# Performance work log

Measured on AMD Instinct MI355X. Metric: run time of the kernel, lower is better.

Reference implementation:

```python
import jax, jax.numpy as jnp
import numpy as np

B, L, D = 4, 4096, 1024
LN_EPS = 1e-5
SCAN_EPS = 1e-8


def setup_inputs() -> dict:
    key = jax.random.key(0)
    ks = jax.random.split(key, 5)
    s = 1.0 / np.sqrt(D)
    return {
        "X": jax.random.normal(ks[0], (B, L, D), dtype=jnp.float32),
        "Wa": jax.random.normal(ks[1], (D, D), dtype=jnp.float32) * s,
        "ba": jnp.zeros((D,), dtype=jnp.float32),
        "Wb": jax.random.normal(ks[2], (D, D), dtype=jnp.float32) * s,
        "bb": jnp.zeros((D,), dtype=jnp.float32),
        "Wc": jax.random.normal(ks[3], (D, D), dtype=jnp.float32) * s,
        "bc": jnp.zeros((D,), dtype=jnp.float32),
        "gamma": jnp.ones((D,), dtype=jnp.float32),
        "beta": jnp.zeros((D,), dtype=jnp.float32),
        "h0": jax.random.normal(ks[4], (1, D), dtype=jnp.float32),
    }


def reference(X, Wa, ba, Wb, bb, Wc, bc, gamma, beta, h0):
    # LayerNorm over last dim
    mu = jnp.mean(X, axis=-1, keepdims=True)
    var = jnp.mean(jnp.square(X - mu), axis=-1, keepdims=True)
    Z = (X - mu) * jax.lax.rsqrt(var + LN_EPS) * gamma + beta  # [B,L,D]

    A = jax.nn.sigmoid(jnp.einsum("bld,ed->ble", Z, Wa) + ba)   # gate in (0,1)
    P = jnp.cumprod(A, axis=1)                                   # decay products
    Bx = jnp.einsum("bld,ed->ble", Z, Wb) + bb
    S = jnp.cumsum(Bx / (P + SCAN_EPS), axis=1)
    # h_t = P_t * h0 + P_t * sum_{s<=t} Bx_s / P_s   (linear recurrence)
    h = P * (h0[:, None, :] + S)                                 # h0 [1,D] broadcasts
    C = jnp.einsum("bld,ed->ble", Z, Wc) + bc
    return C * h + X  # dropout is identity at inference
```

## Files before the change

kernel.cpp:

```cpp
#include <hip/hip_runtime.h>
#include <hip/hip_bf16.h>
#include <cstdint>
#include <cstddef>

#define B_ 4
#define L_ 4096
#define D_ 1024
#define M_ (B_ * L_)
#define LN_EPS 1e-5f
#define SCAN_EPS 1e-8f
#define CT 64
#define NC (L_ / CT)

typedef float f32x4 __attribute__((ext_vector_type(4)));
typedef short bf16x8 __attribute__((ext_vector_type(8)));

__device__ __forceinline__ void gload_lds16(const void* g, void* l) {
    __builtin_amdgcn_global_load_lds(
        (const __attribute__((address_space(1))) void*)g,
        (__attribute__((address_space(3))) void*)l, 16, 0, 0);
}

__global__ __launch_bounds__(256) void ln_kernel(
    const float* __restrict__ X, const float* __restrict__ gamma,
    const float* __restrict__ beta, __hip_bfloat16* __restrict__ Zb)
{
    const int row = blockIdx.x;
    const int tid = threadIdx.x;
    const float* x = X + (size_t)row * D_;

    float4 v = *reinterpret_cast<const float4*>(x + tid * 4);
    float s = v.x + v.y + v.z + v.w;
    #pragma unroll
    for (int off = 32; off > 0; off >>= 1) s += __shfl_down(s, off);

    __shared__ float red[4];
    __shared__ float red2[4];
    const int wid = tid >> 6, lane = tid & 63;
    if (lane == 0) red[wid] = s;
    __syncthreads();
    const float mean = (red[0] + red[1] + red[2] + red[3]) * (1.0f / D_);

    const float dx = v.x - mean, dy = v.y - mean, dz = v.z - mean, dw = v.w - mean;
    float s2 = dx * dx + dy * dy + dz * dz + dw * dw;
    #pragma unroll
    for (int off = 32; off > 0; off >>= 1) s2 += __shfl_down(s2, off);
    if (lane == 0) red2[wid] = s2;
    __syncthreads();
    const float var = (red2[0] + red2[1] + red2[2] + red2[3]) * (1.0f / D_);
    const float rs = rsqrtf(var + LN_EPS);

    float4 g  = *reinterpret_cast<const float4*>(gamma + tid * 4);
    float4 be = *reinterpret_cast<const float4*>(beta + tid * 4);
    union { ushort4 u4; __hip_bfloat16 h[4]; } pk;
    pk.h[0] = __float2bfloat16(dx * rs * g.x + be.x);
    pk.h[1] = __float2bfloat16(dy * rs * g.y + be.y);
    pk.h[2] = __float2bfloat16(dz * rs * g.z + be.z);
    pk.h[3] = __float2bfloat16(dw * rs * g.w + be.w);
    *reinterpret_cast<ushort4*>(Zb + (size_t)row * D_ + tid * 4) = pk.u4;
}

__global__ __launch_bounds__(256) void cvt_w3(
    const float* __restrict__ Wa, const float* __restrict__ Wb,
    const float* __restrict__ Wc, __hip_bfloat16* __restrict__ Wbf)
{
    const int gid = blockIdx.x * 256 + threadIdx.x;
    const size_t i = (size_t)gid * 8;
    const int which = (int)(i >> 20);
    const size_t off = i & ((1ull << 20) - 1);
    const float* W = (which == 0) ? Wa : (which == 1) ? Wb : Wc;
    float4 v0 = *reinterpret_cast<const float4*>(W + off);
    float4 v1 = *reinterpret_cast<const float4*>(W + off + 4);
    union { bf16x8 v; __hip_bfloat16 h[8]; } pk;
    pk.h[0] = __float2bfloat16(v0.x); pk.h[1] = __float2bfloat16(v0.y);
    pk.h[2] = __float2bfloat16(v0.z); pk.h[3] = __float2bfloat16(v0.w);
    pk.h[4] = __float2bfloat16(v1.x); pk.h[5] = __float2bfloat16(v1.y);
    pk.h[6] = __float2bfloat16(v1.z); pk.h[7] = __float2bfloat16(v1.w);
    *reinterpret_cast<bf16x8*>(Wbf + i) = pk.v;
}

#define TM 128
#define TN 128
#define TK 32

__global__ __launch_bounds__(256) void gemm3_mfma(
    const __hip_bfloat16* __restrict__ Zb, const __hip_bfloat16* __restrict__ Wbf,
    const float* __restrict__ ba, const float* __restrict__ bb, const float* __restrict__ bc,
    __hip_bfloat16* __restrict__ Aout, __hip_bfloat16* __restrict__ Bxout,
    __hip_bfloat16* __restrict__ Cout, float* __restrict__ LP)
{
    __shared__ __hip_bfloat16 As[TM * TK];
    __shared__ __hip_bfloat16 Bs[TN * TK];

    const int tid  = threadIdx.x;
    const int wv   = tid >> 6;
    const int lane = tid & 63;
    const int wr   = wv >> 1, wc = wv & 1;
    const int m0   = blockIdx.y * TM;
    const int n0g  = blockIdx.x * TN;
    const int which = n0g >> 10;
    const int n0   = n0g & 1023;

    const __hip_bfloat16* __restrict__ Wsrc = Wbf + ((size_t)which << 20);
    const float* __restrict__ bias = (which == 0) ? ba : (which == 1) ? bb : bc;

    const int c0 = tid, c1 = 256 + tid;
    const int row0 = c0 >> 2, sc0 = (c0 & 3) ^ ((row0 >> 1) & 3);
    const int row1 = c1 >> 2, sc1 = (c1 & 3) ^ ((row1 >> 1) & 3);
    __hip_bfloat16* aDst0 = As + (size_t)(wv * 64) * 8;
    __hip_bfloat16* aDst1 = As + (size_t)(256 + wv * 64) * 8;
    __hip_bfloat16* bDst0 = Bs + (size_t)(wv * 64) * 8;
    __hip_bfloat16* bDst1 = Bs + (size_t)(256 + wv * 64) * 8;

    f32x4 acc[4][4] = {};

    for (int k0 = 0; k0 < D_; k0 += TK) {
        __syncthreads();
        gload_lds16(Zb   + (size_t)(m0 + row0) * D_ + k0 + sc0 * 8, aDst0);
        gload_lds16(Zb   + (size_t)(m0 + row1) * D_ + k0 + sc1 * 8, aDst1);
        gload_lds16(Wsrc + (size_t)(n0 + row0) * D_ + k0 + sc0 * 8, bDst0);
        gload_lds16(Wsrc + (size_t)(n0 + row1) * D_ + k0 + sc1 * 8, bDst1);
        __syncthreads();

        bf16x8 af[4], bfr[4];
        const int rl = lane & 15, kg = lane >> 4;
        #pragma unroll
        for (int i = 0; i < 4; ++i) {
            const int ra = wr * 64 + i * 16 + rl;
            af[i] = *reinterpret_cast<const bf16x8*>(
                reinterpret_cast<const char*>(As) + ra * 64 + ((kg ^ ((ra >> 1) & 3)) << 4));
            const int rb = wc * 64 + i * 16 + rl;
            bfr[i] = *reinterpret_cast<const bf16x8*>(
                reinterpret_cast<const char*>(Bs) + rb * 64 + ((kg ^ ((rb >> 1) & 3)) << 4));
        }
        #pragma unroll
        for (int i = 0; i < 4; ++i)
            #pragma unroll
            for (int j = 0; j < 4; ++j)
                acc[i][j] = __builtin_amdgcn_mfma_f32_16x16x32_bf16(
                    af[i], bfr[j], acc[i][j], 0, 0, 0);
    }

    const int cn = n0 + wc * 64 + (lane & 15);
    float bj[4];
    #pragma unroll
    for (int j = 0; j < 4; ++j) bj[j] = bias[cn + j * 16];

    if (which == 0) {
        float pp[4] = {1.0f, 1.0f, 1.0f, 1.0f};
        #pragma unroll
        for (int i = 0; i < 4; ++i) {
            #pragma unroll
            for (int r = 0; r < 4; ++r) {
                const int m = m0 + wr * 64 + i * 16 + (lane >> 4) * 4 + r;
                __hip_bfloat16* dst = Aout + (size_t)m * D_ + cn;
                #pragma unroll
                for (int j = 0; j < 4; ++j) {
                    const float val = 1.0f / (1.0f + expf(-(acc[i][j][r] + bj[j])));
                    const __hip_bfloat16 hb = __float2bfloat16(val);
                    dst[j * 16] = hb;
                    pp[j] *= __bfloat162float(hb);
                }
            }
        }
        #pragma unroll
        for (int j = 0; j < 4; ++j) {
            pp[j] *= __shfl_xor(pp[j], 16);
            pp[j] *= __shfl_xor(pp[j], 32);
        }
        const int rl = lane & 15, kg = lane >> 4;
        const float sel = (kg == 0) ? pp[0] : (kg == 1) ? pp[1] : (kg == 2) ? pp[2] : pp[3];
        const int bseq = m0 >> 12;
        const int cidx = ((m0 & 4095) >> 6) + wr;
        LP[((size_t)bseq * NC + cidx) * D_ + n0 + wc * 64 + kg * 16 + rl] = sel;
    } else {
        __hip_bfloat16* __restrict__ Out = (which == 1) ? Bxout : Cout;
        #pragma unroll
        for (int i = 0; i < 4; ++i) {
            #pragma unroll
            for (int r = 0; r < 4; ++r) {
                const int m = m0 + wr * 64 + i * 16 + (lane >> 4) * 4 + r;
                __hip_bfloat16* dst = Out + (size_t)m * D_ + cn;
                #pragma unroll
                for (int j = 0; j < 4; ++j)
                    dst[j * 16] = __float2bfloat16(acc[i][j][r] + bj[j]);
            }
        }
    }
}

__global__ __launch_bounds__(256) void scan_chunkpfx(
    const float* __restrict__ LP, float* __restrict__ Pstart)
{
    const int id = blockIdx.x * 256 + threadIdx.x;
    const int e = id & (D_ - 1);
    const int b = id >> 10;
    const size_t base = (size_t)b * NC * D_ + e;
    float p = 1.0f;
    for (int c = 0; c < NC; ++c) {
        Pstart[base + (size_t)c * D_] = p;
        p *= LP[base + (size_t)c * D_];
    }
}

__global__ __launch_bounds__(256) void scan_chunksum(
    const __hip_bfloat16* __restrict__ A, const __hip_bfloat16* __restrict__ Bx,
    const float* __restrict__ Pstart, float* __restrict__ Ssum)
{
    const int id = blockIdx.x * 256 + threadIdx.x;
    const int e = id & (D_ - 1);
    const int c = (id >> 10) & (NC - 1);
    const int b = id >> 16;
    size_t base = ((size_t)b * L_ + (size_t)c * CT) * D_ + e;
    float p = Pstart[id];
    float s = 0.0f;
    #pragma unroll 4
    for (int t = 0; t < CT; ++t) {
        const size_t idx = base + (size_t)t * D_;
        p *= __bfloat162float(A[idx]);
        s += __bfloat162float(Bx[idx]) / (p + SCAN_EPS);
    }
    Ssum[id] = s;
}

__global__ __launch_bounds__(256) void scan_sumpfx(
    const float* __restrict__ Ssum, float* __restrict__ Sstart)
{
    const int id = blockIdx.x * 256 + threadIdx.x;
    const int e = id & (D_ - 1);
    const int b = id >> 10;
    const size_t base = (size_t)b * NC * D_ + e;
    float s = 0.0f;
    for (int c = 0; c < NC; ++c) {
        Sstart[base + (size_t)c * D_] = s;
        s += Ssum[base + (size_t)c * D_];
    }
}

__global__ __launch_bounds__(256) void scan_final(
    const __hip_bfloat16* __restrict__ A, const __hip_bfloat16* __restrict__ Bx,
    const __hip_bfloat16* __restrict__ C, const float* __restrict__ X,
    const float* __restrict__ Pstart, const float* __restrict__ Sstart,
    const float* __restrict__ h0, float* __restrict__ out)
{
    const int id = blockIdx.x * 256 + threadIdx.x;
    const int e = id & (D_ - 1);
    const int c = (id >> 10) & (NC - 1);
    const int b = id >> 16;
    size_t base = ((size_t)b * L_ + (size_t)c * CT) * D_ + e;
    float p = Pstart[id];
    float s = Sstart[id];
    const float h0e = h0[e];
    #pragma unroll 4
    for (int t = 0; t < CT; ++t) {
        const size_t idx = base + (size_t)t * D_;
        p *= __bfloat162float(A[idx]);
        s += __bfloat162float(Bx[idx]) / (p + SCAN_EPS);
        const float h = p * (h0e + s);
        out[idx] = fmaf(__bfloat162float(C[idx]), h, X[idx]);
    }
}

extern "C" void kernel_launch(void* const* d_in, const int* in_sizes, int n_in,
                              void* d_out, int out_size, void* d_ws, size_t ws_size,
                              hipStream_t stream)
{
    const float* X     = (const float*)d_in[0];
    const float* Wa    = (const float*)d_in[1];
    const float* ba    = (const float*)d_in[2];
    const float* Wb    = (const float*)d_in[3];
    const float* bb    = (const float*)d_in[4];
    const float* Wc    = (const float*)d_in[5];
    const float* bc    = (const float*)d_in[6];
    const float* gamma = (const float*)d_in[7];
    const float* beta  = (const float*)d_in[8];
    const float* h0    = (const float*)d_in[9];
    float* out = (float*)d_out;

    const size_t NELT = (size_t)M_ * D_;
    const size_t NCH  = (size_t)B_ * NC * D_;

    __hip_bfloat16* Zb   = (__hip_bfloat16*)d_ws;
    __hip_bfloat16* Wbf  = Zb + NELT;
    __hip_bfloat16* Abf  = Wbf + 3ull * 1024 * 1024;
    __hip_bfloat16* Bxbf = Abf + NELT;
    __hip_bfloat16* Cbf  = Bxbf + NELT;
    float* LP   = (float*)(Cbf + NELT);
    float* Pst  = LP   + NCH;
    float* Ssum = Pst  + NCH;
    float* Sst  = Ssum + NCH;
    (void)ws_size; (void)in_sizes; (void)n_in; (void)out_size;

    cvt_w3<<<1536, 256, 0, stream>>>(Wa, Wb, Wc, Wbf);
    ln_kernel<<<M_, 256, 0, stream>>>(X, gamma, beta, Zb);

    gemm3_mfma<<<dim3(3072 / TN, M_ / TM), 256, 0, stream>>>(
        Zb, Wbf, ba, bb, bc, Abf, Bxbf, Cbf, LP);

    scan_chunkpfx<<<16, 256, 0, stream>>>(LP, Pst);
    scan_chunksum<<<1024, 256, 0, stream>>>(Abf, Bxbf, Pst, Ssum);
    scan_sumpfx<<<16, 256, 0, stream>>>(Ssum, Sst);
    scan_final<<<1024, 256, 0, stream>>>(Abf, Bxbf, Cbf, X, Pst, Sst, h0, out);
}
```

Measured before the change: 352.2 us.

## Double-buffer GEMM LDS, swizzle block order, fuse LN with weight cast, vectorize scans

The GEMM now double-buffers its LDS tiles and prefetches the next K slice before computing the current one, dropping one barrier per iteration. It also remaps a 1D grid so that consecutive blocks are spread across XCD-sized groups. LayerNorm switches to a single-pass sum and sum-of-squares reduction and is merged with the weight-conversion kernel into one launch. The scan kernels process two channels per thread with paired bf16 and float loads and use smaller blocks. The single-pass variance is less numerically robust, and double buffering doubles LDS use per block.

```diff
diff --git a/kernel.cpp b/kernel.cpp
--- a/kernel.cpp
+++ b/kernel.cpp
@@ -21,67 +21,69 @@
         (__attribute__((address_space(3))) void*)l, 16, 0, 0);
 }
 
-__global__ __launch_bounds__(256) void ln_kernel(
+__device__ __forceinline__ float bf2f(unsigned short u) {
+    return __uint_as_float((unsigned)u << 16);
+}
+
+__global__ __launch_bounds__(256) void ln_cvt_kernel(
     const float* __restrict__ X, const float* __restrict__ gamma,
-    const float* __restrict__ beta, __hip_bfloat16* __restrict__ Zb)
-{
+    const float* __restrict__ beta, __hip_bfloat16* __restrict__ Zb,
+    const float* __restrict__ Wa, const float* __restrict__ Wb,
+    const float* __restrict__ Wc, __hip_bfloat16* __restrict__ Wbf)
+{
+    const int tid = threadIdx.x;
+    if (blockIdx.x >= M_) {
+        const int gid = (blockIdx.x - M_) * 256 + tid;
+        const size_t i = (size_t)gid * 8;
+        const int which = (int)(i >> 20);
+        const size_t off = i & ((1ull << 20) - 1);
+        const float* W = (which == 0) ? Wa : (which == 1) ? Wb : Wc;
+        float4 v0 = *reinterpret_cast<const float4*>(W + off);
+        float4 v1 = *reinterpret_cast<const float4*>(W + off + 4);
+        union { bf16x8 v; __hip_bfloat16 h[8]; } pk;
+        pk.h[0] = __float2bfloat16(v0.x); pk.h[1] = __float2bfloat16(v0.y);
+        pk.h[2] = __float2bfloat16(v0.z); pk.h[3] = __float2bfloat16(v0.w);
+        pk.h[4] = __float2bfloat16(v1.x); pk.h[5] = __float2bfloat16(v1.y);
+        pk.h[6] = __float2bfloat16(v1.z); pk.h[7] = __float2bfloat16(v1.w);
+        *reinterpret_cast<bf16x8*>(Wbf + i) = pk.v;
+        return;
+    }
+
     const int row = blockIdx.x;
-    const int tid = threadIdx.x;
     const float* x = X + (size_t)row * D_;
 
     float4 v = *reinterpret_cast<const float4*>(x + tid * 4);
     float s = v.x + v.y + v.z + v.w;
+    float q = v.x * v.x + v.y * v.y + v.z * v.z + v.w * v.w;
     #pragma unroll
-    for (int off = 32; off > 0; off >>= 1) s += __shfl_down(s, off);
-
-    __shared__ float red[4];
-    __shared__ float red2[4];
+    for (int off = 32; off > 0; off >>= 1) {
+        s += __shfl_down(s, off);
+        q += __shfl_down(q, off);
+    }
+
+    __shared__ float red[8];
     const int wid = tid >> 6, lane = tid & 63;
-    if (lane == 0) red[wid] = s;
+    if (lane == 0) { red[wid] = s; red[4 + wid] = q; }
     __syncthreads();
     const float mean = (red[0] + red[1] + red[2] + red[3]) * (1.0f / D_);
-
-    const float dx = v.x - mean, dy = v.y - mean, dz = v.z - mean, dw = v.w - mean;
-    float s2 = dx * dx + dy * dy + dz * dz + dw * dw;
-    #pragma unroll
-    for (int off = 32; off > 0; off >>= 1) s2 += __shfl_down(s2, off);
-    if (lane == 0) red2[wid] = s2;
-    __syncthreads();
-    const float var = (red2[0] + red2[1] + red2[2] + red2[3]) * (1.0f / D_);
+    const float ex2  = (red[4] + red[5] + red[6] + red[7]) * (1.0f / D_);
+    const float var  = ex2 - mean * mean;
     const float rs = rsqrtf(var + LN_EPS);
 
     float4 g  = *reinterpret_cast<const float4*>(gamma + tid * 4);
     float4 be = *reinterpret_cast<const float4*>(beta + tid * 4);
     union { ushort4 u4; __hip_bfloat16 h[4]; } pk;
-    pk.h[0] = __float2bfloat16(dx * rs * g.x + be.x);
-    pk.h[1] = __float2bfloat16(dy * rs * g.y + be.y);
-    pk.h[2] = __float2bfloat16(dz * rs * g.z + be.z);
-    pk.h[3] = __float2bfloat16(dw * rs * g.w + be.w);
+    pk.h[0] = __float2bfloat16((v.x - mean) * rs * g.x + be.x);
+    pk.h[1] = __float2bfloat16((v.y - mean) * rs * g.y + be.y);
+    pk.h[2] = __float2bfloat16((v.z - mean) * rs * g.z + be.z);
+    pk.h[3] = __float2bfloat16((v.w - mean) * rs * g.w + be.w);
     *reinterpret_cast<ushort4*>(Zb + (size_t)row * D_ + tid * 4) = pk.u4;
-}
-
-__global__ __launch_bounds__(256) void cvt_w3(
-    const float* __restrict__ Wa, const float* __restrict__ Wb,
-    const float* __restrict__ Wc, __hip_bfloat16* __restrict__ Wbf)
-{
-    const int gid = blockIdx.x * 256 + threadIdx.x;
-    const size_t i = (size_t)gid * 8;
-    const int which = (int)(i >> 20);
-    const size_t off = i & ((1ull << 20) - 1);
-    const float* W = (which == 0) ? Wa : (which == 1) ? Wb : Wc;
-    float4 v0 = *reinterpret_cast<const float4*>(W + off);
-    float4 v1 = *reinterpret_cast<const float4*>(W + off + 4);
-    union { bf16x8 v; __hip_bfloat16 h[8]; } pk;
-    pk.h[0] = __float2bfloat16(v0.x); pk.h[1] = __float2bfloat16(v0.y);
-    pk.h[2] = __float2bfloat16(v0.z); pk.h[3] = __float2bfloat16(v0.w);
-    pk.h[4] = __float2bfloat16(v1.x); pk.h[5] = __float2bfloat16(v1.y);
-    pk.h[6] = __float2bfloat16(v1.z); pk.h[7] = __float2bfloat16(v1.w);
-    *reinterpret_cast<bf16x8*>(Wbf + i) = pk.v;
 }
 
 #define TM 128
 #define TN 128
 #define TK 32
+#define NKS (D_ / TK)
 
 __global__ __launch_bounds__(256) void gemm3_mfma(
     const __hip_bfloat16* __restrict__ Zb, const __hip_bfloat16* __restrict__ Wbf,
@@ -89,15 +91,20 @@
     __hip_bfloat16* __restrict__ Aout, __hip_bfloat16* __restrict__ Bxout,
     __hip_bfloat16* __restrict__ Cout, float* __restrict__ LP)
 {
-    __shared__ __hip_bfloat16 As[TM * TK];
-    __shared__ __hip_bfloat16 Bs[TN * TK];
+    __shared__ __hip_bfloat16 As[2][TM * TK];
+    __shared__ __hip_bfloat16 Bs[2][TN * TK];
 
     const int tid  = threadIdx.x;
     const int wv   = tid >> 6;
     const int lane = tid & 63;
     const int wr   = wv >> 1, wc = wv & 1;
-    const int m0   = blockIdx.y * TM;
-    const int n0g  = blockIdx.x * TN;
+
+    const int braw = blockIdx.x;
+    const int bid  = (braw & 7) * 384 + (braw >> 3);
+    const int nb   = bid % 24;
+    const int mb   = bid / 24;
+    const int m0   = mb * TM;
+    const int n0g  = nb * TN;
     const int which = n0g >> 10;
     const int n0   = n0g & 1023;
 
@@ -107,31 +114,42 @@
     const int c0 = tid, c1 = 256 + tid;
     const int row0 = c0 >> 2, sc0 = (c0 & 3) ^ ((row0 >> 1) & 3);
     const int row1 = c1 >> 2, sc1 = (c1 & 3) ^ ((row1 >> 1) & 3);
-    __hip_bfloat16* aDst0 = As + (size_t)(wv * 64) * 8;
-    __hip_bfloat16* aDst1 = As + (size_t)(256 + wv * 64) * 8;
-    __hip_bfloat16* bDst0 = Bs + (size_t)(wv * 64) * 8;
-    __hip_bfloat16* bDst1 = Bs + (size_t)(256 + wv * 64) * 8;
+    const int dOff0 = (wv * 64) * 8;
+    const int dOff1 = (256 + wv * 64) * 8;
+    const __hip_bfloat16* zSrc0 = Zb + (size_t)(m0 + row0) * D_ + sc0 * 8;
+    const __hip_bfloat16* zSrc1 = Zb + (size_t)(m0 + row1) * D_ + sc1 * 8;
+    const __hip_bfloat16* wSrc0 = Wsrc + (size_t)(n0 + row0) * D_ + sc0 * 8;
+    const __hip_bfloat16* wSrc1 = Wsrc + (size_t)(n0 + row1) * D_ + sc1 * 8;
 
     f32x4 acc[4][4] = {};
-
-    for (int k0 = 0; k0 < D_; k0 += TK) {
-        __syncthreads();
-        gload_lds16(Zb   + (size_t)(m0 + row0) * D_ + k0 + sc0 * 8, aDst0);
-        gload_lds16(Zb   + (size_t)(m0 + row1) * D_ + k0 + sc1 * 8, aDst1);
-        gload_lds16(Wsrc + (size_t)(n0 + row0) * D_ + k0 + sc0 * 8, bDst0);
-        gload_lds16(Wsrc + (size_t)(n0 + row1) * D_ + k0 + sc1 * 8, bDst1);
-        __syncthreads();
-
+    const int rl = lane & 15, kg = lane >> 4;
+
+    gload_lds16(zSrc0, &As[0][dOff0]);
+    gload_lds16(zSrc1, &As[0][dOff1]);
+    gload_lds16(wSrc0, &Bs[0][dOff0]);
+    gload_lds16(wSrc1, &Bs[0][dOff1]);
+    __syncthreads();
+
+    int cur = 0;
+    for (int t = 0; t < NKS; ++t) {
+        if (t < NKS - 1) {
+            const int k1 = (t + 1) * TK;
+            gload_lds16(zSrc0 + k1, &As[cur ^ 1][dOff0]);
+            gload_lds16(zSrc1 + k1, &As[cur ^ 1][dOff1]);
+            gload_lds16(wSrc0 + k1, &Bs[cur ^ 1][dOff0]);
+            gload_lds16(wSrc1 + k1, &Bs[cur ^ 1][dOff1]);
+        }
         bf16x8 af[4], bfr[4];
-        const int rl = lane & 15, kg = lane >> 4;
+        const char* aBase = reinterpret_cast<const char*>(As[cur]);
+        const char* bBase = reinterpret_cast<const char*>(Bs[cur]);
         #pragma unroll
         for (int i = 0; i < 4; ++i) {
             const int ra = wr * 64 + i * 16 + rl;
             af[i] = *reinterpret_cast<const bf16x8*>(
-                reinterpret_cast<const char*>(As) + ra * 64 + ((kg ^ ((ra >> 1) & 3)) << 4));
+                aBase + ra * 64 + ((kg ^ ((ra >> 1) & 3)) << 4));
             const int rb = wc * 64 + i * 16 + rl;
             bfr[i] = *reinterpret_cast<const bf16x8*>(
-                reinterpret_cast<const char*>(Bs) + rb * 64 + ((kg ^ ((rb >> 1) & 3)) << 4));
+                bBase + rb * 64 + ((kg ^ ((rb >> 1) & 3)) << 4));
         }
         #pragma unroll
         for (int i = 0; i < 4; ++i)
@@ -139,9 +157,11 @@
             for (int j = 0; j < 4; ++j)
                 acc[i][j] = __builtin_amdgcn_mfma_f32_16x16x32_bf16(
                     af[i], bfr[j], acc[i][j], 0, 0, 0);
-    }
-
-    const int cn = n0 + wc * 64 + (lane & 15);
+        __syncthreads();
+        cur ^= 1;
+    }
+
+    const int cn = n0 + wc * 64 + rl;
     float bj[4];
     #pragma unroll
     for (int j = 0; j < 4; ++j) bj[j] = bias[cn + j * 16];
@@ -152,7 +172,7 @@
         for (int i = 0; i < 4; ++i) {
             #pragma unroll
             for (int r = 0; r < 4; ++r) {
-                const int m = m0 + wr * 64 + i * 16 + (lane >> 4) * 4 + r;
+                const int m = m0 + wr * 64 + i * 16 + kg * 4 + r;
                 __hip_bfloat16* dst = Aout + (size_t)m * D_ + cn;
                 #pragma unroll
                 for (int j = 0; j < 4; ++j) {
@@ -168,7 +188,6 @@
             pp[j] *= __shfl_xor(pp[j], 16);
             pp[j] *= __shfl_xor(pp[j], 32);
         }
-        const int rl = lane & 15, kg = lane >> 4;
         const float sel = (kg == 0) ? pp[0] : (kg == 1) ? pp[1] : (kg == 2) ? pp[2] : pp[3];
         const int bseq = m0 >> 12;
         const int cidx = ((m0 & 4095) >> 6) + wr;
@@ -179,7 +198,7 @@
         for (int i = 0; i < 4; ++i) {
             #pragma unroll
             for (int r = 0; r < 4; ++r) {
-                const int m = m0 + wr * 64 + i * 16 + (lane >> 4) * 4 + r;
+                const int m = m0 + wr * 64 + i * 16 + kg * 4 + r;
                 __hip_bfloat16* dst = Out + (size_t)m * D_ + cn;
                 #pragma unroll
                 for (int j = 0; j < 4; ++j)
@@ -189,75 +208,87 @@
     }
 }
 
-__global__ __launch_bounds__(256) void scan_chunkpfx(
+__global__ __launch_bounds__(128) void scan_chunkpfx(
     const float* __restrict__ LP, float* __restrict__ Pstart)
 {
-    const int id = blockIdx.x * 256 + threadIdx.x;
-    const int e = id & (D_ - 1);
-    const int b = id >> 10;
+    const int ch = blockIdx.x * 128 + threadIdx.x;
+    const int e = ch & (D_ - 1);
+    const int b = ch >> 10;
     const size_t base = (size_t)b * NC * D_ + e;
     float p = 1.0f;
+    #pragma unroll 8
     for (int c = 0; c < NC; ++c) {
         Pstart[base + (size_t)c * D_] = p;
         p *= LP[base + (size_t)c * D_];
     }
 }
 
-__global__ __launch_bounds__(256) void scan_chunksum(
+__global__ __launch_bounds__(128) void scan_chunksum(
     const __hip_bfloat16* __restrict__ A, const __hip_bfloat16* __restrict__ Bx,
     const float* __restrict__ Pstart, float* __restrict__ Ssum)
 {
-    const int id = blockIdx.x * 256 + threadIdx.x;
-    const int e = id & (D_ - 1);
-    const int c = (id >> 10) & (NC - 1);
-    const int b = id >> 16;
+    const int blk = blockIdx.x;
+    const int eg = blk & 3, c = (blk >> 2) & (NC - 1), b = blk >> 8;
+    const int e = eg * 256 + threadIdx.x * 2;
     size_t base = ((size_t)b * L_ + (size_t)c * CT) * D_ + e;
-    float p = Pstart[id];
-    float s = 0.0f;
+    const size_t chid = ((size_t)b * NC + c) * D_ + e;
+    float2 pst = *reinterpret_cast<const float2*>(Pstart + chid);
+    float p0 = pst.x, p1 = pst.y, s0 = 0.0f, s1 = 0.0f;
     #pragma unroll 4
     for (int t = 0; t < CT; ++t) {
         const size_t idx = base + (size_t)t * D_;
-        p *= __bfloat162float(A[idx]);
-        s += __bfloat162float(Bx[idx]) / (p + SCAN_EPS);
-    }
-    Ssum[id] = s;
-}
-
-__global__ __launch_bounds__(256) void scan_sumpfx(
+        ushort2 a  = *reinterpret_cast<const ushort2*>(A + idx);
+        ushort2 bx = *reinterpret_cast<const ushort2*>(Bx + idx);
+        p0 *= bf2f(a.x);  p1 *= bf2f(a.y);
+        s0 += bf2f(bx.x) / (p0 + SCAN_EPS);
+        s1 += bf2f(bx.y) / (p1 + SCAN_EPS);
+    }
+    *reinterpret_cast<float2*>(Ssum + chid) = make_float2(s0, s1);
+}
+
+__global__ __launch_bounds__(128) void scan_sumpfx(
     const float* __restrict__ Ssum, float* __restrict__ Sstart)
 {
-    const int id = blockIdx.x * 256 + threadIdx.x;
-    const int e = id & (D_ - 1);
-    const int b = id >> 10;
+    const int ch = blockIdx.x * 128 + threadIdx.x;
+    const int e = ch & (D_ - 1);
+    const int b = ch >> 10;
     const size_t base = (size_t)b * NC * D_ + e;
     float s = 0.0f;
+    #pragma unroll 8
     for (int c = 0; c < NC; ++c) {
         Sstart[base + (size_t)c * D_] = s;
         s += Ssum[base + (size_t)c * D_];
     }
 }
 
-__global__ __launch_bounds__(256) void scan_final(
+__global__ __launch_bounds__(128) void scan_final(
     const __hip_bfloat16* __restrict__ A, const __hip_bfloat16* __restrict__ Bx,
     const __hip_bfloat16* __restrict__ C, const float* __restrict__ X,
     const float* __restrict__ Pstart, const float* __restrict__ Sstart,
     const float* __restrict__ h0, float* __restrict__ out)
 {
-    const int id = blockIdx.x * 256 + threadIdx.x;
-    const int e = id & (D_ - 1);
-    const int c = (id >> 10) & (NC - 1);
-    const int b = id >> 16;
+    const int blk = blockIdx.x;
+    const int eg = blk & 3, c = (blk >> 2) & (NC - 1), b = blk >> 8;
+    const int e = eg * 256 + threadIdx.x * 2;
     size_t base = ((size_t)b * L_ + (size_t)c * CT) * D_ + e;
-    float p = Pstart[id];
-    float s = Sstart[id];
-    const float h0e = h0[e];
+    const size_t chid = ((size_t)b * NC + c) * D_ + e;
+    float2 pst = *reinterpret_cast<const float2*>(Pstart + chid);
+    float2 sst = *reinterpret_cast<const float2*>(Sstart + chid);
+    float2 h02 = *reinterpret_cast<const float2*>(h0 + e);
+    float p0 = pst.x, p1 = pst.y, s0 = sst.x, s1 = sst.y;
     #pragma unroll 4
     for (int t = 0; t < CT; ++t) {
         const size_t idx = base + (size_t)t * D_;
-        p *= __bfloat162float(A[idx]);
-        s += __bfloat162float(Bx[idx]) / (p + SCAN_EPS);
-        const float h = p * (h0e + s);
-        out[idx] = fmaf(__bfloat162float(C[idx]), h, X[idx]);
+        ushort2 a  = *reinterpret_cast<const ushort2*>(A + idx);
+        ushort2 bx = *reinterpret_cast<const ushort2*>(Bx + idx);
+        ushort2 cc = *reinterpret_cast<const ushort2*>(C + idx);
+        float2 x   = *reinterpret_cast<const float2*>(X + idx);
+        p0 *= bf2f(a.x);  p1 *= bf2f(a.y);
+        s0 += bf2f(bx.x) / (p0 + SCAN_EPS);
+        s1 += bf2f(bx.y) / (p1 + SCAN_EPS);
+        const float o0 = fmaf(bf2f(cc.x), p0 * (h02.x + s0), x.x);
+        const float o1 = fmaf(bf2f(cc.y), p1 * (h02.y + s1), x.y);
+        *reinterpret_cast<float2*>(out + idx) = make_float2(o0, o1);
     }
 }
 
@@ -291,14 +322,13 @@
     float* Sst  = Ssum + NCH;
     (void)ws_size; (void)in_sizes; (void)n_in; (void)out_size;
 
-    cvt_w3<<<1536, 256, 0, stream>>>(Wa, Wb, Wc, Wbf);
-    ln_kernel<<<M_, 256, 0, stream>>>(X, gamma, beta, Zb);
-
-    gemm3_mfma<<<dim3(3072 / TN, M_ / TM), 256, 0, stream>>>(
+    ln_cvt_kernel<<<M_ + 1536, 256, 0, stream>>>(X, gamma, beta, Zb, Wa, Wb, Wc, Wbf);
+
+    gemm3_mfma<<<3072, 256, 0, stream>>>(
         Zb, Wbf, ba, bb, bc, Abf, Bxbf, Cbf, LP);
 
-    scan_chunkpfx<<<16, 256, 0, stream>>>(LP, Pst);
-    scan_chunksum<<<1024, 256, 0, stream>>>(Abf, Bxbf, Pst, Ssum);
-    scan_sumpfx<<<16, 256, 0, stream>>>(Ssum, Sst);
-    scan_final<<<1024, 256, 0, stream>>>(Abf, Bxbf, Cbf, X, Pst, Sst, h0, out);
-}
+    scan_chunkpfx<<<32, 128, 0, stream>>>(LP, Pst);
+    scan_chunksum<<<1024, 128, 0, stream>>>(Abf, Bxbf, Pst, Ssum);
+    scan_sumpfx<<<32, 128, 0, stream>>>(Ssum, Sst);
+    scan_final<<<1024, 128, 0, stream>>>(Abf, Bxbf, Cbf, X, Pst, Sst, h0, out);
+}
```

Result: no change. 357.8 us (+1.6%).
